# Kernel optimization log

Measured on AMD Instinct MI355X. Metric: run time of the kernel, lower is better.

## Reference

```python
import jax, jax.numpy as jnp
import numpy as np

N = 50000      # nodes
E = 1600000    # edges (before self loops)
IN = 128
OUT = 128
H = 4
HD = OUT // H  # head dim = 32


def setup_inputs() -> dict:
    key = jax.random.key(0)
    k1, k2, k3, k4, k5 = jax.random.split(key, 5)
    x = jax.random.normal(k1, (N, IN), dtype=jnp.float32)
    edge_index = jax.random.randint(k2, (2, E), 0, N, dtype=jnp.int64)
    # xavier-uniform-ish scales
    W = jax.random.normal(k3, (OUT, IN), dtype=jnp.float32) * (1.0 / np.sqrt(IN))
    att_src = jax.random.normal(k4, (1, H, HD), dtype=jnp.float32) * 0.1
    att_dst = jax.random.normal(k5, (1, H, HD), dtype=jnp.float32) * 0.1
    return {"x": x, "edge_index": edge_index, "W": W, "att_src": att_src, "att_dst": att_dst}


def reference(x, edge_index, W, att_src, att_dst):
    n = x.shape[0]
    # add self loops (tg.utils.add_self_loops appends [i, i] edges)
    loops = jnp.arange(n, dtype=edge_index.dtype)
    ei = jnp.concatenate([edge_index, jnp.stack([loops, loops])], axis=1)
    src, dst = ei[0], ei[1]

    # linear projection, split into heads: [n, H, HD]
    h = (x @ W.T).reshape(n, H, HD)

    # per-node attention logits per head: [n, H]
    a_src = jnp.sum(h * att_src, axis=-1)
    a_dst = jnp.sum(h * att_dst, axis=-1)

    # per-edge attention score: gather + leaky_relu
    alpha = a_src[src] + a_dst[dst]                      # [Etot, H]
    alpha = jax.nn.leaky_relu(alpha, negative_slope=0.2)

    # segment softmax grouped by destination node (numerically stable)
    m = jax.ops.segment_max(alpha, dst, num_segments=n)  # [n, H]
    e = jnp.exp(alpha - m[dst])
    s = jax.ops.segment_sum(e, dst, num_segments=n)      # [n, H]
    e = e / s[dst]                                       # [Etot, H]

    # weighted scatter-add aggregation; f_additive adds 1 to the weights
    msg = h[src] * (e[:, :, None] + 1.0)                 # [Etot, H, HD]
    out = jax.ops.segment_sum(msg, dst, num_segments=n)  # [n, H, HD]
    return out.reshape(n, -1)
```

## Files before the change

### kernel.cpp

```cpp
#include <hip/hip_runtime.h>

#define N_NODES 50000
#define E_EDGES 1600000
#define ETOT    (E_EDGES + N_NODES)
#define DIN  128
#define DOUT 128
#define NH   4
#define HD   32

typedef unsigned short ushort_t;
typedef unsigned int uint_t;
typedef __attribute__((ext_vector_type(8))) short bfrag;
typedef __attribute__((ext_vector_type(4))) float ffrag;

__device__ __forceinline__ ushort_t f2bf(float f) {
  uint_t u = __float_as_uint(f);
  u += 0x7fffu + ((u >> 16) & 1u);
  return (ushort_t)(u >> 16);
}
__device__ __forceinline__ float bf_lo(uint_t u) {
  return __uint_as_float(u << 16);
}
__device__ __forceinline__ float bf_hi(uint_t u) {
  return __uint_as_float(u & 0xffff0000u);
}

#define BSZ   64
#define NBUCK ((N_NODES + BSZ - 1) / BSZ)
#define CAP   2560
#define EPB_A 4096
#define NBLK_A ((ETOT + EPB_A - 1) / EPB_A)
#define NCHUNK 13

__global__ __launch_bounds__(256, 4) void fused_binA_gemm_kernel(
    const int* __restrict__ ei, int* __restrict__ gcur,
    uint_t* __restrict__ ebuf,
    const float* __restrict__ x, const float* __restrict__ W,
    const float* __restrict__ att_src, const float* __restrict__ att_dst,
    ushort_t* __restrict__ hb, float* __restrict__ a_src,
    float* __restrict__ a_dst) {
  __shared__ ushort_t Ws[DIN * DOUT];
  const int tid = threadIdx.x;

  if (blockIdx.x < NBLK_A) {
    int* hist = (int*)Ws;
    int* base = hist + NBUCK;
    const int e0 = blockIdx.x * EPB_A;
    const int e1 = min(e0 + EPB_A, ETOT);
    for (int i = tid; i < NBUCK; i += 256) hist[i] = 0;
    __syncthreads();
    for (int e = e0 + tid; e < e1; e += 256) {
      int di = (e < E_EDGES) ? ei[E_EDGES + e] : (e - E_EDGES);
      atomicAdd(&hist[di >> 6], 1);
    }
    __syncthreads();
    for (int i = tid; i < NBUCK; i += 256) {
      int c = hist[i];
      base[i] = (c > 0) ? (i * CAP + atomicAdd(&gcur[i], c)) : 0;
      hist[i] = 0;
    }
    __syncthreads();
    for (int e = e0 + tid; e < e1; e += 256) {
      int si, di;
      if (e < E_EDGES) { si = ei[e]; di = ei[E_EDGES + e]; }
      else             { si = e - E_EDGES; di = si; }
      int b = di >> 6;
      int pos = base[b] + atomicAdd(&hist[b], 1);
      if (pos < (b + 1) * CAP)
        ebuf[pos] = ((uint_t)(di & 63) << 24) | (uint_t)si;
    }
    return;
  }

  const int gb = blockIdx.x - NBLK_A;
  const int wv = tid >> 6, l = tid & 63;
  const int lr = l & 15, lg = l >> 4;
  const int nbase = gb * 64 + wv * 16;
  int na = nbase + lr;
  if (na >= N_NODES) na = N_NODES - 1;
  const float* xrow = x + (size_t)na * DIN;

  float4 px[8];
#pragma unroll
  for (int kt = 0; kt < 4; kt++) {
    px[kt * 2]     = *(const float4*)&xrow[kt * 32 + lg * 8];
    px[kt * 2 + 1] = *(const float4*)&xrow[kt * 32 + lg * 8 + 4];
  }

  for (int u = tid; u < 2048; u += 256) {
    int row = u >> 4;
    float4 w0 = *(const float4*)&W[u * 8];
    float4 w1 = *(const float4*)&W[u * 8 + 4];
    uint4 pk;
    pk.x = (uint_t)f2bf(w0.x) | ((uint_t)f2bf(w0.y) << 16);
    pk.y = (uint_t)f2bf(w0.z) | ((uint_t)f2bf(w0.w) << 16);
    pk.z = (uint_t)f2bf(w1.x) | ((uint_t)f2bf(w1.y) << 16);
    pk.w = (uint_t)f2bf(w1.z) | ((uint_t)f2bf(w1.w) << 16);
    *(uint4*)&Ws[(u ^ (row & 7)) * 8] = pk;
  }
  __syncthreads();

  ffrag acc[8];
#pragma unroll
  for (int oc = 0; oc < 8; oc++) acc[oc] = (ffrag){0.f, 0.f, 0.f, 0.f};

#pragma unroll
  for (int kt = 0; kt < 4; kt++) {
    const float4 x0 = px[kt * 2];
    const float4 x1 = px[kt * 2 + 1];
    bfrag a;
    a[0] = (short)f2bf(x0.x); a[1] = (short)f2bf(x0.y);
    a[2] = (short)f2bf(x0.z); a[3] = (short)f2bf(x0.w);
    a[4] = (short)f2bf(x1.x); a[5] = (short)f2bf(x1.y);
    a[6] = (short)f2bf(x1.z); a[7] = (short)f2bf(x1.w);
#pragma unroll
    for (int oc = 0; oc < 8; oc++) {
      const int u = ((oc * 16 + lr) << 4) + kt * 4 + lg;
      const bfrag b = *(const bfrag*)&Ws[(u ^ (lr & 7)) * 8];
      acc[oc] = __builtin_amdgcn_mfma_f32_16x16x32_bf16(a, b, acc[oc], 0, 0, 0);
    }
  }

#pragma unroll
  for (int oc = 0; oc < 8; oc++) {
#pragma unroll
    for (int j = 0; j < 4; j++) {
      int n = nbase + lg * 4 + j;
      if (n < N_NODES)
        hb[((size_t)n << 7) + oc * 16 + lr] = f2bf(acc[oc][j]);
    }
  }

  float asv[8], adv[8];
#pragma unroll
  for (int oc = 0; oc < 8; oc++) {
    asv[oc] = att_src[oc * 16 + lr];
    adv[oc] = att_dst[oc * 16 + lr];
  }
#pragma unroll
  for (int j = 0; j < 4; j++) {
    float ps[4] = {0.f, 0.f, 0.f, 0.f};
    float pd[4] = {0.f, 0.f, 0.f, 0.f};
#pragma unroll
    for (int oc = 0; oc < 8; oc++) {
      ps[oc >> 1] = fmaf(acc[oc][j], asv[oc], ps[oc >> 1]);
      pd[oc >> 1] = fmaf(acc[oc][j], adv[oc], pd[oc >> 1]);
    }
#pragma unroll
    for (int off = 1; off < 16; off <<= 1) {
#pragma unroll
      for (int hd = 0; hd < 4; hd++) {
        ps[hd] += __shfl_xor(ps[hd], off);
        pd[hd] += __shfl_xor(pd[hd], off);
      }
    }
    int n = nbase + lg * 4 + j;
    if (n < N_NODES && lr < 4) {
      float vs = lr == 0 ? ps[0] : lr == 1 ? ps[1] : lr == 2 ? ps[2] : ps[3];
      float vd = lr == 0 ? pd[0] : lr == 1 ? pd[1] : lr == 2 ? pd[2] : pd[3];
      a_src[n * NH + lr] = vs;
      a_dst[n * NH + lr] = vd;
    }
  }
}

__global__ __launch_bounds__(256) void binB_kernel(
    const uint_t* __restrict__ ebuf, const int* __restrict__ gcur,
    int* __restrict__ rs, int* __restrict__ re, int* __restrict__ col) {
  __shared__ int cnt[BSZ * NCHUNK];
  __shared__ int roff[BSZ * NCHUNK];
  const int b = blockIdx.x;
  const int tid = threadIdx.x;
  const int n0 = b << 6;
  const int nn = min(BSZ, N_NODES - n0);
  const int s0 = b * CAP;
  const int s1 = s0 + min(gcur[b], CAP);
  for (int k = tid; k < BSZ * NCHUNK; k += 256) cnt[k] = 0;
  __syncthreads();
  for (int i = s0 + tid; i < s1; i += 256) {
    uint_t p = ebuf[i];
    int key = (int)(p >> 24) * NCHUNK + (int)((p & 0xFFFFFFu) >> 12);
    atomicAdd(&cnt[key], 1);
  }
  __syncthreads();
  if (tid < BSZ) {
    int pref[NCHUNK];
    int tot = 0;
#pragma unroll
    for (int k = 0; k < NCHUNK; k++) { pref[k] = tot; tot += cnt[tid * NCHUNK + k]; }
    int xx = tot;
#pragma unroll
    for (int off = 1; off < 64; off <<= 1) {
      int y = __shfl_up(xx, off, 64);
      if (tid >= off) xx += y;
    }
    const int nodebase = xx - tot;
#pragma unroll
    for (int k = 0; k < NCHUNK; k++) roff[tid * NCHUNK + k] = nodebase + pref[k];
    if (tid < nn) {
      rs[n0 + tid] = s0 + nodebase;
      re[n0 + tid] = s0 + nodebase + tot;
    }
  }
  __syncthreads();
  for (int k = tid; k < BSZ * NCHUNK; k += 256) cnt[k] = 0;
  __syncthreads();
  for (int i = s0 + tid; i < s1; i += 256) {
    uint_t p = ebuf[i];
    int si = (int)(p & 0xFFFFFFu);
    int key = (int)(p >> 24) * NCHUNK + (si >> 12);
    int pos = atomicAdd(&cnt[key], 1);
    int q = s0 + roff[key] + pos;
    if (q >= 0 && q < NBUCK * CAP) col[q] = si;
  }
}

#define NPB 16
#define CH  16

__global__ __launch_bounds__(256, 8) void agg_kernel(
    const int* __restrict__ col, const int* __restrict__ rs,
    const int* __restrict__ re, const ushort_t* __restrict__ hb,
    const float* __restrict__ a_src, const float* __restrict__ a_dst,
    float* __restrict__ out) {
  __shared__ float w_lds[NPB][CH][NH];
  __shared__ int   si_lds[NPB][CH];
  const int tid  = threadIdx.x;
  const int slot = tid >> 4;
  const int t    = tid & 15;
  const int node = blockIdx.x * NPB + slot;
  const int start = rs[node];
  const int deg   = re[node] - start;
  const float4 ad = *(const float4*)(a_dst + (size_t)node * NH);

  const int head = t >> 2;
  const int c8 = t << 3;
  const ushort_t* hc = hb + c8;
  float s = 0.f;
  float a0 = 0.f, a1 = 0.f, a2 = 0.f, a3 = 0.f;
  float a4 = 0.f, a5 = 0.f, a6 = 0.f, a7 = 0.f;
  float b0 = 0.f, b1 = 0.f, b2 = 0.f, b3 = 0.f;
  float b4 = 0.f, b5 = 0.f, b6 = 0.f, b7 = 0.f;

  for (int base_e = 0; base_e < deg; base_e += CH) {
    int nch = deg - base_e;
    if (nch > CH) nch = CH;
    if (t < nch) {
      int si = col[start + base_e + t];
      si = si < N_NODES ? si : 0;
      si_lds[slot][t] = si;
      float4 as = *(const float4*)(a_src + (size_t)si * NH);
      float v0 = as.x + ad.x; v0 = v0 > 0.f ? v0 : 0.2f * v0;
      float v1 = as.y + ad.y; v1 = v1 > 0.f ? v1 : 0.2f * v1;
      float v2 = as.z + ad.z; v2 = v2 > 0.f ? v2 : 0.2f * v2;
      float v3 = as.w + ad.w; v3 = v3 > 0.f ? v3 : 0.2f * v3;
      w_lds[slot][t][0] = __expf(v0);
      w_lds[slot][t][1] = __expf(v1);
      w_lds[slot][t][2] = __expf(v2);
      w_lds[slot][t][3] = __expf(v3);
    }
    __builtin_amdgcn_fence(__ATOMIC_ACQ_REL, "wavefront");
#pragma unroll 2
    for (int j = 0; j < nch; j++) {
      int si = si_lds[slot][j];
      float e = w_lds[slot][j][head];
      s += e;
      const uint4 hv = *(const uint4*)(hc + ((size_t)si << 7));
      float h0 = bf_lo(hv.x), h1 = bf_hi(hv.x);
      float h2 = bf_lo(hv.y), h3 = bf_hi(hv.y);
      float h4 = bf_lo(hv.z), h5 = bf_hi(hv.z);
      float h6 = bf_lo(hv.w), h7 = bf_hi(hv.w);
      a0 = fmaf(h0, e, a0); b0 += h0;
      a1 = fmaf(h1, e, a1); b1 += h1;
      a2 = fmaf(h2, e, a2); b2 += h2;
      a3 = fmaf(h3, e, a3); b3 += h3;
      a4 = fmaf(h4, e, a4); b4 += h4;
      a5 = fmaf(h5, e, a5); b5 += h5;
      a6 = fmaf(h6, e, a6); b6 += h6;
      a7 = fmaf(h7, e, a7); b7 += h7;
    }
    __builtin_amdgcn_fence(__ATOMIC_ACQ_REL, "wavefront");
  }
  const float inv = 1.0f / s;
  float* op = out + ((size_t)node << 7) + c8;
  *(float4*)(op)     = make_float4(fmaf(a0, inv, b0), fmaf(a1, inv, b1),
                                   fmaf(a2, inv, b2), fmaf(a3, inv, b3));
  *(float4*)(op + 4) = make_float4(fmaf(a4, inv, b4), fmaf(a5, inv, b5),
                                   fmaf(a6, inv, b6), fmaf(a7, inv, b7));
}

extern "C" void kernel_launch(void* const* d_in, const int* in_sizes, int n_in,
                              void* d_out, int out_size, void* d_ws, size_t ws_size,
                              hipStream_t stream) {
  const float* x       = (const float*)d_in[0];
  const int*   ei      = (const int*)d_in[1];
  const float* W       = (const float*)d_in[2];
  const float* att_src = (const float*)d_in[3];
  const float* att_dst = (const float*)d_in[4];
  float* out = (float*)d_out;

  ushort_t* hb = (ushort_t*)d_ws;
  float* a_src = (float*)(hb + (size_t)N_NODES * DOUT);
  float* a_dst = a_src + (size_t)N_NODES * NH;
  int* gcur    = (int*)(a_dst + (size_t)N_NODES * NH);
  int* rs      = gcur + NBUCK;
  int* re      = rs + N_NODES;
  int* col     = re + N_NODES;
  uint_t* ebuf = (uint_t*)(col + (size_t)NBUCK * CAP);

  hipMemsetAsync(gcur, 0, (size_t)NBUCK * sizeof(int), stream);

  const int gemm_blocks = (N_NODES + 63) / 64;
  fused_binA_gemm_kernel<<<NBLK_A + gemm_blocks, 256, 0, stream>>>(
      ei, gcur, ebuf, x, W, att_src, att_dst, hb, a_src, a_dst);
  binB_kernel<<<NBUCK, 256, 0, stream>>>(ebuf, gcur, rs, re, col);
  agg_kernel<<<N_NODES / NPB, 256, 0, stream>>>(col, rs, re, hb, a_src, a_dst, out);
}
```

Before: 105.6 us.

## Replace global atomic bucket reservation with count, scan, and deterministic placement passes

Edge binning is split into a per-block histogram written to a count matrix (fused with the GEMM kernel), a per-bucket scan kernel that computes each block's offset, and a separate placement kernel. This drops the global atomicAdd reservations and the memset, and makes edge order within buckets deterministic. Edges per block are doubled so the count matrix stays small enough for a 64-lane scan. The cost is two extra kernel launches and a second read of the edge index.

```diff
diff --git a/kernel.cpp b/kernel.cpp
--- a/kernel.cpp
+++ b/kernel.cpp
@@ -28,24 +28,24 @@
 #define BSZ   64
 #define NBUCK ((N_NODES + BSZ - 1) / BSZ)
 #define CAP   2560
-#define EPB_A 4096
+#define EPB_A 8192
 #define NBLK_A ((ETOT + EPB_A - 1) / EPB_A)
 #define NCHUNK 13
-
-__global__ __launch_bounds__(256, 4) void fused_binA_gemm_kernel(
-    const int* __restrict__ ei, int* __restrict__ gcur,
-    uint_t* __restrict__ ebuf,
+#define GEMM_BLOCKS ((N_NODES + 63) / 64)
+
+__global__ __launch_bounds__(256, 4) void fused_gemm_count_kernel(
     const float* __restrict__ x, const float* __restrict__ W,
     const float* __restrict__ att_src, const float* __restrict__ att_dst,
     ushort_t* __restrict__ hb, float* __restrict__ a_src,
-    float* __restrict__ a_dst) {
+    float* __restrict__ a_dst,
+    const int* __restrict__ ei, int* __restrict__ cnt) {
   __shared__ ushort_t Ws[DIN * DOUT];
   const int tid = threadIdx.x;
 
-  if (blockIdx.x < NBLK_A) {
+  if (blockIdx.x >= GEMM_BLOCKS) {
     int* hist = (int*)Ws;
-    int* base = hist + NBUCK;
-    const int e0 = blockIdx.x * EPB_A;
+    const int cb = blockIdx.x - GEMM_BLOCKS;
+    const int e0 = cb * EPB_A;
     const int e1 = min(e0 + EPB_A, ETOT);
     for (int i = tid; i < NBUCK; i += 256) hist[i] = 0;
     __syncthreads();
@@ -54,25 +54,12 @@
       atomicAdd(&hist[di >> 6], 1);
     }
     __syncthreads();
-    for (int i = tid; i < NBUCK; i += 256) {
-      int c = hist[i];
-      base[i] = (c > 0) ? (i * CAP + atomicAdd(&gcur[i], c)) : 0;
-      hist[i] = 0;
-    }
-    __syncthreads();
-    for (int e = e0 + tid; e < e1; e += 256) {
-      int si, di;
-      if (e < E_EDGES) { si = ei[e]; di = ei[E_EDGES + e]; }
-      else             { si = e - E_EDGES; di = si; }
-      int b = di >> 6;
-      int pos = base[b] + atomicAdd(&hist[b], 1);
-      if (pos < (b + 1) * CAP)
-        ebuf[pos] = ((uint_t)(di & 63) << 24) | (uint_t)si;
-    }
+    for (int i = tid; i < NBUCK; i += 256)
+      cnt[(size_t)cb * NBUCK + i] = hist[i];
     return;
   }
 
-  const int gb = blockIdx.x - NBLK_A;
+  const int gb = blockIdx.x;
   const int wv = tid >> 6, l = tid & 63;
   const int lr = l & 15, lg = l >> 4;
   const int nbase = gb * 64 + wv * 16;
@@ -164,30 +151,81 @@
   }
 }
 
+__global__ __launch_bounds__(64) void bscan_kernel(
+    int* __restrict__ cnt, int* __restrict__ btot) {
+  const int b = blockIdx.x;
+  const int lane = threadIdx.x;
+  const int blk = lane * 4;
+  int v0 = 0, v1 = 0, v2 = 0, v3 = 0;
+  if (blk     < NBLK_A) v0 = cnt[(size_t)blk * NBUCK + b];
+  if (blk + 1 < NBLK_A) v1 = cnt[(size_t)(blk + 1) * NBUCK + b];
+  if (blk + 2 < NBLK_A) v2 = cnt[(size_t)(blk + 2) * NBUCK + b];
+  if (blk + 3 < NBLK_A) v3 = cnt[(size_t)(blk + 3) * NBUCK + b];
+  const int p1 = v0, p2 = v0 + v1, p3 = v0 + v1 + v2;
+  const int s = v0 + v1 + v2 + v3;
+  int xx = s;
+#pragma unroll
+  for (int off = 1; off < 64; off <<= 1) {
+    int y = __shfl_up(xx, off, 64);
+    if (lane >= off) xx += y;
+  }
+  const int base = b * CAP + (xx - s);
+  if (blk     < NBLK_A) cnt[(size_t)blk * NBUCK + b]       = base;
+  if (blk + 1 < NBLK_A) cnt[(size_t)(blk + 1) * NBUCK + b] = base + p1;
+  if (blk + 2 < NBLK_A) cnt[(size_t)(blk + 2) * NBUCK + b] = base + p2;
+  if (blk + 3 < NBLK_A) cnt[(size_t)(blk + 3) * NBUCK + b] = base + p3;
+  if (lane == 63) btot[b] = xx;
+}
+
+__global__ __launch_bounds__(256) void place_kernel(
+    const int* __restrict__ ei, const int* __restrict__ cnt,
+    uint_t* __restrict__ ebuf) {
+  __shared__ int base[NBUCK];
+  __shared__ int hist[NBUCK];
+  const int cb = blockIdx.x;
+  const int tid = threadIdx.x;
+  for (int i = tid; i < NBUCK; i += 256) {
+    base[i] = cnt[(size_t)cb * NBUCK + i];
+    hist[i] = 0;
+  }
+  __syncthreads();
+  const int e0 = cb * EPB_A;
+  const int e1 = min(e0 + EPB_A, ETOT);
+  for (int e = e0 + tid; e < e1; e += 256) {
+    int si, di;
+    if (e < E_EDGES) { si = ei[e]; di = ei[E_EDGES + e]; }
+    else             { si = e - E_EDGES; di = si; }
+    int b = di >> 6;
+    int pos = base[b] + atomicAdd(&hist[b], 1);
+    if (pos < (b + 1) * CAP)
+      ebuf[pos] = ((uint_t)(di & 63) << 24) | (uint_t)si;
+  }
+}
+
 __global__ __launch_bounds__(256) void binB_kernel(
-    const uint_t* __restrict__ ebuf, const int* __restrict__ gcur,
+    const uint_t* __restrict__ ebuf, const int* __restrict__ btot,
     int* __restrict__ rs, int* __restrict__ re, int* __restrict__ col) {
-  __shared__ int cnt[BSZ * NCHUNK];
+  __shared__ int cnt_l[BSZ * NCHUNK];
   __shared__ int roff[BSZ * NCHUNK];
   const int b = blockIdx.x;
   const int tid = threadIdx.x;
   const int n0 = b << 6;
   const int nn = min(BSZ, N_NODES - n0);
   const int s0 = b * CAP;
-  const int s1 = s0 + min(gcur[b], CAP);
-  for (int k = tid; k < BSZ * NCHUNK; k += 256) cnt[k] = 0;
+  const int s1 = s0 + min(btot[b], CAP);
+  for (int k = tid; k < BSZ * NCHUNK; k += 256) cnt_l[k] = 0;
   __syncthreads();
   for (int i = s0 + tid; i < s1; i += 256) {
     uint_t p = ebuf[i];
     int key = (int)(p >> 24) * NCHUNK + (int)((p & 0xFFFFFFu) >> 12);
-    atomicAdd(&cnt[key], 1);
+    atomicAdd(&cnt_l[key], 1);
   }
   __syncthreads();
   if (tid < BSZ) {
     int pref[NCHUNK];
     int tot = 0;
 #pragma unroll
-    for (int k = 0; k < NCHUNK; k++) { pref[k] = tot; tot += cnt[tid * NCHUNK + k]; }
+    for (int k = 0; k < NCHUNK; k++) { pref[k] = tot; tot += cnt_l[tid * NCHUNK + k]; }
     int xx = tot;
 #pragma unroll
     for (int off = 1; off < 64; off <<= 1) {
@@ -203,13 +241,13 @@
     }
   }
   __syncthreads();
-  for (int k = tid; k < BSZ * NCHUNK; k += 256) cnt[k] = 0;
+  for (int k = tid; k < BSZ * NCHUNK; k += 256) cnt_l[k] = 0;
   __syncthreads();
   for (int i = s0 + tid; i < s1; i += 256) {
     uint_t p = ebuf[i];
     int si = (int)(p & 0xFFFFFFu);
     int key = (int)(p >> 24) * NCHUNK + (si >> 12);
-    int pos = atomicAdd(&cnt[key], 1);
+    int pos = atomicAdd(&cnt_l[key], 1);
     int q = s0 + roff[key] + pos;
     if (q >= 0 && q < NBUCK * CAP) col[q] = si;
   }
@@ -302,17 +340,17 @@
   ushort_t* hb = (ushort_t*)d_ws;
   float* a_src = (float*)(hb + (size_t)N_NODES * DOUT);
   float* a_dst = a_src + (size_t)N_NODES * NH;
-  int* gcur    = (int*)(a_dst + (size_t)N_NODES * NH);
-  int* rs      = gcur + NBUCK;
+  int* cnt     = (int*)(a_dst + (size_t)N_NODES * NH);
+  int* btot    = cnt + (size_t)NBLK_A * NBUCK;
+  int* rs      = btot + NBUCK;
   int* re      = rs + N_NODES;
   int* col     = re + N_NODES;
   uint_t* ebuf = (uint_t*)(col + (size_t)NBUCK * CAP);
 
-  hipMemsetAsync(gcur, 0, (size_t)NBUCK * sizeof(int), stream);
-
-  const int gemm_blocks = (N_NODES + 63) / 64;
-  fused_binA_gemm_kernel<<<NBLK_A + gemm_blocks, 256, 0, stream>>>(
-      ei, gcur, ebuf, x, W, att_src, att_dst, hb, a_src, a_dst);
-  binB_kernel<<<NBUCK, 256, 0, stream>>>(ebuf, gcur, rs, re, col);
+  fused_gemm_count_kernel<<<GEMM_BLOCKS + NBLK_A, 256, 0, stream>>>(
+      x, W, att_src, att_dst, hb, a_src, a_dst, ei, cnt);
+  bscan_kernel<<<NBUCK, 64, 0, stream>>>(cnt, btot);
+  place_kernel<<<NBLK_A, 256, 0, stream>>>(ei, cnt, ebuf);
+  binB_kernel<<<NBUCK, 256, 0, stream>>>(ebuf, btot, rs, re, col);
   agg_kernel<<<N_NODES / NPB, 256, 0, stream>>>(col, rs, re, hb, a_src, a_dst, out);
 }
```

Result: slower. 108.9 us (+3.1%).

## Replace global-atomic edge binning with per-block local sort and count matrix

Applied to the files above, without the earlier changes.

Each edge-binning block now stages its 8192 edges in LDS, builds a per-bucket histogram and prefix scan, and writes its edges sorted by bucket into its own contiguous region of ebuf. It records per-block bucket counts and offsets in a matrix, so the global atomic counters and the memset are no longer needed. binB then scans that matrix column for its bucket, gathers each block's segment into LDS, and sorts from LDS rather than rereading ebuf twice. This aims to cut global atomics and scattered writes. The cost is a serial per-thread gather loop in binB and a packed 16-bit src/dst encoding, which holds only because N is below 65536.

```diff
diff --git a/kernel.cpp b/kernel.cpp
--- a/kernel.cpp
+++ b/kernel.cpp
@@ -27,51 +27,87 @@
 
 #define BSZ   64
 #define NBUCK ((N_NODES + BSZ - 1) / BSZ)
+#define NBP   1024
 #define CAP   2560
-#define EPB_A 4096
+#define EPB_A 8192
 #define NBLK_A ((ETOT + EPB_A - 1) / EPB_A)
 #define NCHUNK 13
 
+
 __global__ __launch_bounds__(256, 4) void fused_binA_gemm_kernel(
-    const int* __restrict__ ei, int* __restrict__ gcur,
-    uint_t* __restrict__ ebuf,
+    const int* __restrict__ ei, uint_t* __restrict__ ebuf,
+    int* __restrict__ cntm, int* __restrict__ offm,
     const float* __restrict__ x, const float* __restrict__ W,
     const float* __restrict__ att_src, const float* __restrict__ att_dst,
     ushort_t* __restrict__ hb, float* __restrict__ a_src,
     float* __restrict__ a_dst) {
-  __shared__ ushort_t Ws[DIN * DOUT];
+  __shared__ uint_t lds[EPB_A + NBP + 8];
   const int tid = threadIdx.x;
 
   if (blockIdx.x < NBLK_A) {
-    int* hist = (int*)Ws;
-    int* base = hist + NBUCK;
-    const int e0 = blockIdx.x * EPB_A;
-    const int e1 = min(e0 + EPB_A, ETOT);
-    for (int i = tid; i < NBUCK; i += 256) hist[i] = 0;
-    __syncthreads();
-    for (int e = e0 + tid; e < e1; e += 256) {
-      int di = (e < E_EDGES) ? ei[E_EDGES + e] : (e - E_EDGES);
-      atomicAdd(&hist[di >> 6], 1);
-    }
-    __syncthreads();
-    for (int i = tid; i < NBUCK; i += 256) {
-      int c = hist[i];
-      base[i] = (c > 0) ? (i * CAP + atomicAdd(&gcur[i], c)) : 0;
-      hist[i] = 0;
-    }
-    __syncthreads();
-    for (int e = e0 + tid; e < e1; e += 256) {
+    uint_t* stage = lds;
+    int* hist = (int*)(lds + EPB_A);
+    int* wsum = hist + NBP;
+    const int cb = blockIdx.x;
+    const int e0 = cb * EPB_A;
+    const int n = min(EPB_A, ETOT - e0);
+    for (int i = tid; i < NBP; i += 256) hist[i] = 0;
+    __syncthreads();
+    for (int i = tid; i < n; i += 256) {
+      int e = e0 + i;
       int si, di;
       if (e < E_EDGES) { si = ei[e]; di = ei[E_EDGES + e]; }
       else             { si = e - E_EDGES; di = si; }
-      int b = di >> 6;
-      int pos = base[b] + atomicAdd(&hist[b], 1);
-      if (pos < (b + 1) * CAP)
-        ebuf[pos] = ((uint_t)(di & 63) << 24) | (uint_t)si;
+      stage[i] = ((uint_t)di << 16) | (uint_t)si;
+      atomicAdd(&hist[di >> 6], 1);
+    }
+    __syncthreads();
+    const int ln = tid & 63, wv = tid >> 6;
+    int c0 = hist[4 * tid], c1 = hist[4 * tid + 1];
+    int c2 = hist[4 * tid + 2], c3 = hist[4 * tid + 3];
+    int p1 = c0, p2 = c0 + c1, p3 = c0 + c1 + c2;
+    int tot = p3 + c3;
+    int xx = tot;
+#pragma unroll
+    for (int off = 1; off < 64; off <<= 1) {
+      int y = __shfl_up(xx, off, 64);
+      if (ln >= off) xx += y;
+    }
+    if (ln == 63) wsum[wv] = xx;
+    __syncthreads();
+    if (tid < 4) {
+      int w = wsum[tid];
+#pragma unroll
+      for (int off = 1; off < 4; off <<= 1) {
+        int y = __shfl_up(w, off, 64);
+        if (tid >= off) w += y;
+      }
+      wsum[tid] = w;
+    }
+    __syncthreads();
+    const int wo = (wv == 0) ? 0 : wsum[wv - 1];
+    const int base = wo + xx - tot;
+#pragma unroll
+    for (int k = 0; k < 4; k++) {
+      int idx = 4 * tid + k;
+      int c = k == 0 ? c0 : k == 1 ? c1 : k == 2 ? c2 : c3;
+      int o = base + (k == 0 ? 0 : k == 1 ? p1 : k == 2 ? p2 : p3);
+      if (idx < NBUCK) {
+        cntm[(size_t)cb * NBP + idx] = c;
+        offm[(size_t)cb * NBP + idx] = o;
+      }
+      hist[idx] = o;
+    }
+    __syncthreads();
+    for (int i = tid; i < n; i += 256) {
+      uint_t p = stage[i];
+      int pos = atomicAdd(&hist[p >> 22], 1);
+      if (pos >= 0 && pos < n) ebuf[e0 + pos] = p;
     }
     return;
   }
 
+  ushort_t* Ws = (ushort_t*)lds;
   const int gb = blockIdx.x - NBLK_A;
   const int wv = tid >> 6, l = tid & 63;
   const int lr = l & 15, lg = l >> 4;
@@ -165,52 +201,87 @@
 }
 
 __global__ __launch_bounds__(256) void binB_kernel(
-    const uint_t* __restrict__ ebuf, const int* __restrict__ gcur,
+    const uint_t* __restrict__ ebuf, const int* __restrict__ cntm,
+    const int* __restrict__ offm,
     int* __restrict__ rs, int* __restrict__ re, int* __restrict__ col) {
-  __shared__ int cnt[BSZ * NCHUNK];
-  __shared__ int roff[BSZ * NCHUNK];
+  __shared__ uint_t el[CAP];
+  __shared__ int cnt_l[BSZ * NCHUNK];
+  __shared__ int roff_l[BSZ * NCHUNK];
+  __shared__ int wsum[4];
   const int b = blockIdx.x;
   const int tid = threadIdx.x;
+  const int ln = tid & 63, wv = tid >> 6;
   const int n0 = b << 6;
   const int nn = min(BSZ, N_NODES - n0);
-  const int s0 = b * CAP;
-  const int s1 = s0 + min(gcur[b], CAP);
-  for (int k = tid; k < BSZ * NCHUNK; k += 256) cnt[k] = 0;
-  __syncthreads();
-  for (int i = s0 + tid; i < s1; i += 256) {
-    uint_t p = ebuf[i];
-    int key = (int)(p >> 24) * NCHUNK + (int)((p & 0xFFFFFFu) >> 12);
-    atomicAdd(&cnt[key], 1);
+
+  int c = (tid < NBLK_A) ? cntm[(size_t)tid * NBP + b] : 0;
+  int o = (tid < NBLK_A) ? offm[(size_t)tid * NBP + b] : 0;
+  int xx = c;
+#pragma unroll
+  for (int off = 1; off < 64; off <<= 1) {
+    int y = __shfl_up(xx, off, 64);
+    if (ln >= off) xx += y;
+  }
+  if (ln == 63) wsum[wv] = xx;
+  __syncthreads();
+  if (tid < 4) {
+    int w = wsum[tid];
+#pragma unroll
+    for (int off = 1; off < 4; off <<= 1) {
+      int y = __shfl_up(w, off, 64);
+      if (tid >= off) w += y;
+    }
+    wsum[tid] = w;
+  }
+  __syncthreads();
+  const int wo = (wv == 0) ? 0 : wsum[wv - 1];
+  const int mystart = wo + xx - c;
+  const int total0 = wsum[3];
+  const int total = total0 < CAP ? total0 : CAP;
+  if (tid < NBLK_A) {
+    const uint_t* src = ebuf + (size_t)tid * EPB_A + o;
+    for (int j = 0; j < c; j++) {
+      int d = mystart + j;
+      if (d < CAP) el[d] = src[j];
+    }
+  }
+  for (int k = tid; k < BSZ * NCHUNK; k += 256) cnt_l[k] = 0;
+  __syncthreads();
+
+  for (int i = tid; i < total; i += 256) {
+    uint_t p = el[i];
+    int key = (int)((p >> 16) & 63) * NCHUNK + (int)((p & 0xFFFFu) >> 12);
+    atomicAdd(&cnt_l[key], 1);
   }
   __syncthreads();
   if (tid < BSZ) {
     int pref[NCHUNK];
     int tot = 0;
 #pragma unroll
-    for (int k = 0; k < NCHUNK; k++) { pref[k] = tot; tot += cnt[tid * NCHUNK + k]; }
-    int xx = tot;
+    for (int k = 0; k < NCHUNK; k++) { pref[k] = tot; tot += cnt_l[tid * NCHUNK + k]; }
+    int x2 = tot;
 #pragma unroll
     for (int off = 1; off < 64; off <<= 1) {
-      int y = __shfl_up(xx, off, 64);
-      if (tid >= off) xx += y;
-    }
-    const int nodebase = xx - tot;
-#pragma unroll
-    for (int k = 0; k < NCHUNK; k++) roff[tid * NCHUNK + k] = nodebase + pref[k];
+      int y = __shfl_up(x2, off, 64);
+      if (tid >= off) x2 += y;
+    }
+    const int nodebase = x2 - tot;
+#pragma unroll
+    for (int k = 0; k < NCHUNK; k++) roff_l[tid * NCHUNK + k] = nodebase + pref[k];
     if (tid < nn) {
-      rs[n0 + tid] = s0 + nodebase;
-      re[n0 + tid] = s0 + nodebase + tot;
-    }
-  }
-  __syncthreads();
-  for (int k = tid; k < BSZ * NCHUNK; k += 256) cnt[k] = 0;
-  __syncthreads();
-  for (int i = s0 + tid; i < s1; i += 256) {
-    uint_t p = ebuf[i];
-    int si = (int)(p & 0xFFFFFFu);
-    int key = (int)(p >> 24) * NCHUNK + (si >> 12);
-    int pos = atomicAdd(&cnt[key], 1);
-    int q = s0 + roff[key] + pos;
+      rs[n0 + tid] = b * CAP + nodebase;
+      re[n0 + tid] = b * CAP + nodebase + tot;
+    }
+  }
+  __syncthreads();
+  for (int k = tid; k < BSZ * NCHUNK; k += 256) cnt_l[k] = 0;
+  __syncthreads();
+  for (int i = tid; i < total; i += 256) {
+    uint_t p = el[i];
+    int si = (int)(p & 0xFFFFu);
+    int key = (int)((p >> 16) & 63) * NCHUNK + (si >> 12);
+    int pos = atomicAdd(&cnt_l[key], 1);
+    int q = b * CAP + roff_l[key] + pos;
     if (q >= 0 && q < NBUCK * CAP) col[q] = si;
   }
 }
@@ -302,17 +373,16 @@
   ushort_t* hb = (ushort_t*)d_ws;
   float* a_src = (float*)(hb + (size_t)N_NODES * DOUT);
   float* a_dst = a_src + (size_t)N_NODES * NH;
-  int* gcur    = (int*)(a_dst + (size_t)N_NODES * NH);
-  int* rs      = gcur + NBUCK;
+  int* cntm    = (int*)(a_dst + (size_t)N_NODES * NH);
+  int* offm    = cntm + (size_t)NBLK_A * NBP;
+  int* rs      = offm + (size_t)NBLK_A * NBP;
   int* re      = rs + N_NODES;
   int* col     = re + N_NODES;
   uint_t* ebuf = (uint_t*)(col + (size_t)NBUCK * CAP);
 
-  hipMemsetAsync(gcur, 0, (size_t)NBUCK * sizeof(int), stream);
-
   const int gemm_blocks = (N_NODES + 63) / 64;
   fused_binA_gemm_kernel<<<NBLK_A + gemm_blocks, 256, 0, stream>>>(
-      ei, gcur, ebuf, x, W, att_src, att_dst, hb, a_src, a_dst);
-  binB_kernel<<<NBUCK, 256, 0, stream>>>(ebuf, gcur, rs, re, col);
+      ei, ebuf, cntm, offm, x, W, att_src, att_dst, hb, a_src, a_dst);
+  binB_kernel<<<NBUCK, 256, 0, stream>>>(ebuf, cntm, offm, rs, re, col);
   agg_kernel<<<N_NODES / NPB, 256, 0, stream>>>(col, rs, re, hb, a_src, a_dst, out);
 }
```

New measurement: 103.0 us. 1.03x faster.
